# Performance work log

Measured on AMD Instinct MI355X. Metric: run time of the kernel, lower is better.

Reference implementation:

```python
import jax, jax.numpy as jnp
import numpy as np

B, N1, N2, C2, K = 8, 2048, 128, 256, 3
D_POS, H0, H1 = 32, 512, 1024


def setup_inputs() -> dict:
    key = jax.random.key(0)
    ks = jax.random.split(key, 14)
    return {
        "xyz1": jax.random.normal(ks[0], (B, N1, 3), jnp.float32),
        "xyz2": jax.random.normal(ks[1], (B, N2, 3), jnp.float32),
        "feat2": jax.random.normal(ks[2], (B, N2, C2), jnp.float32),
        "lrf2": jax.random.normal(ks[3], (B, N2, 3, 3), jnp.float32),
        "w_pos": jax.random.normal(ks[4], (D_POS, 4), jnp.float32) * 0.1,
        "pos_scale": jax.random.uniform(ks[5], (D_POS,), jnp.float32, 0.5, 1.5),
        "pos_bias": jax.random.normal(ks[6], (D_POS,), jnp.float32) * 0.1,
        "w0": jax.random.normal(ks[7], (H0, C2 + D_POS), jnp.float32) * 0.05,
        "s0": jax.random.uniform(ks[8], (H0,), jnp.float32, 0.5, 1.5),
        "b0": jax.random.normal(ks[9], (H0,), jnp.float32) * 0.1,
        "w1": jax.random.normal(ks[10], (H1, H0), jnp.float32) * 0.04,
        "s1": jax.random.uniform(ks[11], (H1,), jnp.float32, 0.5, 1.5),
        "b1": jax.random.normal(ks[12], (H1,), jnp.float32) * 0.1,
        "k": K,
    }


def reference(xyz1, xyz2, feat2, lrf2, w_pos, pos_scale, pos_bias,
              w0, s0, b0, w1, s1, b1, k):
    Bb = xyz1.shape[0]
    # --- get_dists: full pairwise sqrt-distance matrix (B, N1, N2) ---
    d2 = (jnp.sum(xyz1 * xyz1, -1)[:, :, None]
          + jnp.sum(xyz2 * xyz2, -1)[:, None, :]
          - 2.0 * jnp.einsum('bmc,bnc->bmn', xyz1, xyz2))
    dists = jnp.sqrt(jnp.where(d2 < 0, 1e-7, d2))
    # --- k-NN: smallest k in ascending order (== torch.sort then slice) ---
    _, inds = jax.lax.top_k(-dists, k)                    # (B, N1, k)
    bidx = jnp.arange(Bb)[:, None, None]
    feat_nb = feat2[bidx, inds]                           # (B, N1, k, C2)
    close = xyz2[bidx, inds]                              # (B, N1, k, 3)
    lrf_nb = lrf2[bidx, inds]                             # (B, N1, k, 3, 3)
    # --- geometric angle embedding ---
    rel = xyz1[:, :, None, :] - close                     # (B, N1, k, 3)
    rel_norm = jnp.linalg.norm(rel, axis=-1)              # (B, N1, k)
    unit = rel / jnp.maximum(rel_norm, 1e-12)[..., None]  # F.normalize eps
    angle = jnp.einsum('bnkij,bnkj->bnki', lrf_nb, unit)  # (B, N1, k, 3)
    rp = jnp.concatenate([rel_norm[..., None], angle], -1)  # (B, N1, k, 4)
    # --- posembed: 1x1 Conv2d (no bias) + folded BN + LeakyReLU(0.2) ---
    pos = jax.nn.leaky_relu(
        jnp.einsum('bnkc,oc->bnko', rp, w_pos) * pos_scale + pos_bias, 0.2)
    # --- backbone: two 1x1 convs with folded BN + ReLU ---
    x = jnp.concatenate([feat_nb, pos], -1)               # (B, N1, k, C2+32)
    h0 = jax.nn.relu(jnp.einsum('bnkc,oc->bnko', x, w0) * s0 + b0)
    h1 = jax.nn.relu(jnp.einsum('bnkc,oc->bnko', h0, w1) * s1 + b1)
    # --- sum over neighbors, return (B, C_out, N1) like torch ---
    return jnp.transpose(jnp.sum(h1, axis=2), (0, 2, 1))
```

## Files before the change

kernel.cpp:

```cpp
#include <hip/hip_runtime.h>


typedef unsigned short u16;
typedef __bf16 bf16x8 __attribute__((ext_vector_type(8)));
typedef float f32x4 __attribute__((ext_vector_type(4)));
typedef u16 u16x4 __attribute__((ext_vector_type(4)));
typedef u16 u16x8 __attribute__((ext_vector_type(8)));

#define BQ 8
#define N1Q 2048
#define N2Q 128
#define C2Q 256
#define DPOS 32
#define H0Q 512
#define H1Q 1024
#define NQ (BQ * N1Q)

#define WS_W0F 0u
#define WS_W0P 262144u
#define WS_W1 294912u
#define WS_F2B 1343488u
#define WS_F 1867776u
#define WS_H0 3964928u
#define WS_POS 54296576u
#define WS_IDX 57442304u

__device__ __forceinline__ u16 f2bf(float f) {
  unsigned int u = __builtin_bit_cast(unsigned int, f);
  return (u16)((u + 0x7FFFu + ((u >> 16) & 1u)) >> 16);
}

__device__ __forceinline__ void load16_lds(const void* g, void* l) {
  __builtin_amdgcn_global_load_lds(
      (const __attribute__((address_space(1))) unsigned int*)g,
      (__attribute__((address_space(3))) unsigned int*)l, 16, 0, 0);
}

__global__ void convert_inputs(const float* __restrict__ w0,
                               const float* __restrict__ w1,
                               const float* __restrict__ feat2,
                               u16* __restrict__ w0f, u16* __restrict__ w0p,
                               u16* __restrict__ w1b, u16* __restrict__ f2b) {
  int i = blockIdx.x * 256 + threadIdx.x;
  if (i < 131072) {
    int h = i >> 8, c = i & 255;
    w0f[i] = f2bf(w0[h * 288 + c]);
  } else if (i < 147456) {
    int j = i - 131072;
    int h = j >> 5, c = j & 31;
    w0p[j] = f2bf(w0[h * 288 + 256 + c]);
  } else if (i < 671744) {
    int j = i - 147456;
    w1b[j] = f2bf(w1[j]);
  } else {
    int j = i - 671744;
    f2b[j] = f2bf(feat2[j]);
  }
}

__global__ __launch_bounds__(256, 2) void fgemm(const u16* __restrict__ A,
                                                const u16* __restrict__ W,
                                                float* __restrict__ F) {
  __shared__ alignas(16) u16 As[128 * 32];
  __shared__ alignas(16) u16 Bs[128 * 32];
  const int m0 = (blockIdx.x >> 2) * 128, n0 = (blockIdx.x & 3) * 128;
  const int t = threadIdx.x;
  const int wv = t >> 6, lane = t & 63;
  const int wm = wv >> 1, wn = wv & 1;
  const int quad = lane >> 4, cc = lane & 15;
  const int srow = lane & 15, skc = quad * 8;
  f32x4 acc[4][4] = {};

  for (int k0 = 0; k0 < 256; k0 += 32) {
#pragma unroll
    for (int i = 0; i < 2; i++) {
      int g = i * 4 + wv;
      load16_lds(A + (size_t)(m0 + g * 16 + srow) * 256 + k0 + skc,
                 (char*)As + g * 1024 + (lane << 4));
      load16_lds(W + (size_t)(n0 + g * 16 + srow) * 256 + k0 + skc,
                 (char*)Bs + g * 1024 + (lane << 4));
    }
    __syncthreads();
    bf16x8 af[4], bf[4];
#pragma unroll
    for (int mt = 0; mt < 4; mt++)
      af[mt] = *(const bf16x8*)((const char*)As + (wm * 4 + mt) * 1024 + (lane << 4));
#pragma unroll
    for (int nt = 0; nt < 4; nt++)
      bf[nt] = *(const bf16x8*)((const char*)Bs + (wn * 4 + nt) * 1024 + (lane << 4));
#pragma unroll
    for (int mt = 0; mt < 4; mt++)
#pragma unroll
      for (int nt = 0; nt < 4; nt++)
        acc[mt][nt] = __builtin_amdgcn_mfma_f32_16x16x32_bf16(
            af[mt], bf[nt], acc[mt][nt], 0, 0, 0);
    __syncthreads();
  }

#pragma unroll
  for (int nt = 0; nt < 4; nt++) {
    int gn = n0 + wn * 64 + nt * 16 + cc;
#pragma unroll
    for (int mt = 0; mt < 4; mt++) {
      int gm = m0 + wm * 64 + mt * 16 + quad * 4;
#pragma unroll
      for (int r = 0; r < 4; r++)
        F[(size_t)(gm + r) * H0Q + gn] = acc[mt][nt][r];
    }
  }
}

__global__ __launch_bounds__(512, 2) void knn_pos(
    const float* __restrict__ xyz1, const float* __restrict__ xyz2,
    const float* __restrict__ lrf2, const float* __restrict__ w_pos,
    const float* __restrict__ pscale, const float* __restrict__ pbias,
    u16* __restrict__ posw, int* __restrict__ idxw) {
  __shared__ float xyz2s[N2Q * 3];
  __shared__ float n2s[N2Q];
  __shared__ float lrfs[N2Q * 9];
  __shared__ float wps[DPOS * 4];
  __shared__ float pss[DPOS];
  __shared__ float pbs[DPOS];
  __shared__ float candd[128 * 13];
  __shared__ int candi[128 * 13];
  __shared__ int idxb[384];

  const int t = threadIdx.x;
  const int qb = blockIdx.x * 128;
  const int b = qb >> 11;

  for (int i = t; i < N2Q * 3; i += 512) xyz2s[i] = xyz2[b * N2Q * 3 + i];
  for (int i = t; i < N2Q * 9; i += 512) lrfs[i] = lrf2[b * N2Q * 9 + i];
  if (t < DPOS * 4) wps[t] = w_pos[t];
  if (t < DPOS) { pss[t] = pscale[t]; pbs[t] = pbias[t]; }
  __syncthreads();
  if (t < N2Q) {
    float x = xyz2s[t * 3], y = xyz2s[t * 3 + 1], z = xyz2s[t * 3 + 2];
    n2s[t] = x * x + y * y + z * z;
  }
  __syncthreads();

  {
    const int ql = t >> 2, qt = t & 3;
    const int q = qb + ql;
    const float px = xyz1[q * 3], py = xyz1[q * 3 + 1], pz = xyz1[q * 3 + 2];
    const float pn = px * px + py * py + pz * pz;
    float d0 = 1e30f, d1 = 1e30f, d2v = 1e30f;
    int i0 = 0, i1 = 0, i2 = 0;
    const int ibeg = qt * 32;
    for (int i = ibeg; i < ibeg + 32; i++) {
      float dt = px * xyz2s[i * 3] + py * xyz2s[i * 3 + 1] + pz * xyz2s[i * 3 + 2];
      float d = pn + n2s[i] - 2.f * dt;
      if (d < d0) {
        d2v = d1; i2 = i1; d1 = d0; i1 = i0; d0 = d; i0 = i;
      } else if (d < d1) {
        d2v = d1; i2 = i1; d1 = d; i1 = i;
      } else if (d < d2v) {
        d2v = d; i2 = i;
      }
    }
    int base = ql * 13 + qt * 3;
    candd[base] = d0;      candi[base] = i0;
    candd[base + 1] = d1;  candi[base + 1] = i1;
    candd[base + 2] = d2v; candi[base + 2] = i2;
  }
  __syncthreads();

  if (t < 128) {
    float d0 = 1e30f, d1 = 1e30f, d2v = 1e30f;
    int i0 = 0, i1 = 0, i2 = 0;
    int base = t * 13;
#pragma unroll
    for (int c = 0; c < 12; c++) {
      float d = candd[base + c];
      int id = candi[base + c];
      if (d < d0) {
        d2v = d1; i2 = i1; d1 = d0; i1 = i0; d0 = d; i0 = id;
      } else if (d < d1) {
        d2v = d1; i2 = i1; d1 = d; i1 = id;
      } else if (d < d2v) {
        d2v = d; i2 = id;
      }
    }
    idxb[t] = i0;
    idxb[128 + t] = i1;
    idxb[256 + t] = i2;
  }
  __syncthreads();

  if (t < 384) {
    const int j = t >> 7, ql = t & 127;
    const int q = qb + ql;
    const float px = xyz1[q * 3], py = xyz1[q * 3 + 1], pz = xyz1[q * 3 + 2];
    const int id = idxb[j * 128 + ql];
    float rx = px - xyz2s[id * 3];
    float ry = py - xyz2s[id * 3 + 1];
    float rz = pz - xyz2s[id * 3 + 2];
    float rn = sqrtf(rx * rx + ry * ry + rz * rz);
    float inv = 1.f / fmaxf(rn, 1e-12f);
    float ux = rx * inv, uy = ry * inv, uz = rz * inv;
    const float* L = lrfs + id * 9;
    float a0 = L[0] * ux + L[1] * uy + L[2] * uz;
    float a1 = L[3] * ux + L[4] * uy + L[5] * uz;
    float a2 = L[6] * ux + L[7] * uy + L[8] * uz;
    const size_t row = (size_t)j * NQ + q;
    idxw[row] = id;
#pragma unroll
    for (int c = 0; c < 4; c++) {
      u16x8 chunk;
#pragma unroll
      for (int e = 0; e < 8; e++) {
        int o = c * 8 + e;
        float v = wps[o * 4] * rn + wps[o * 4 + 1] * a0 + wps[o * 4 + 2] * a1 +
                  wps[o * 4 + 3] * a2;
        v = v * pss[o] + pbs[o];
        v = (v >= 0.f) ? v : 0.2f * v;
        chunk[e] = f2bf(v);
      }
      *(u16x8*)(posw + row * 32 + c * 8) = chunk;
    }
  }
}

__global__ __launch_bounds__(256, 4) void h0_kernel(
    const u16* __restrict__ posw, const int* __restrict__ idxw,
    const u16* __restrict__ w0p, const float* __restrict__ F,
    const float* __restrict__ s0, const float* __restrict__ b0,
    u16* __restrict__ H0) {
  const int t = threadIdx.x;
  const int wv = t >> 6, lane = t & 63;
  const int quad = lane >> 4, cc = lane & 15;
  const int r0 = (blockIdx.x * 4 + wv) * 16;

  const int r = r0 + cc;
  const int q = r & (NQ - 1);
  const int bb = q >> 11;
  const int idv = idxw[r];
  const float* Fr = F + ((size_t)(bb * N2Q + idv)) * H0Q;
  u16* Hr = H0 + (size_t)r * H0Q;

  const bf16x8 afr = *(const bf16x8*)(posw + (size_t)r * 32 + quad * 8);
  const f32x4 zf = {};

#pragma unroll 4
  for (int nt = 0; nt < 32; nt++) {
    const bf16x8 bfr = *(const bf16x8*)(w0p + (nt * 16 + cc) * 32 + quad * 8);
    f32x4 acc = __builtin_amdgcn_mfma_f32_16x16x32_bf16(bfr, afr, zf, 0, 0, 0);
    const int hb = nt * 16 + quad * 4;
    const f32x4 sv = *(const f32x4*)(s0 + hb);
    const f32x4 bv = *(const f32x4*)(b0 + hb);
    const f32x4 fv = *(const f32x4*)(Fr + hb);
    u16x4 o4;
#pragma unroll
    for (int e = 0; e < 4; e++) {
      float h = (fv[e] + acc[e]) * sv[e] + bv[e];
      h = h > 0.f ? h : 0.f;
      o4[e] = f2bf(h);
    }
    *(u16x4*)(Hr + hb) = o4;
  }
}

__global__ __launch_bounds__(512, 2) void gemm2(const u16* __restrict__ A,
                                                const u16* __restrict__ W,
                                                const float* __restrict__ s,
                                                const float* __restrict__ bz,
                                                float* __restrict__ out) {
  __shared__ alignas(16) u16 As[3][128 * 64];
  __shared__ alignas(16) u16 Bs[3][256 * 64];
  const int id = blockIdx.x;
  const int xcd = id & 7, g = id >> 3;
  const int m0 = (xcd * 16 + (g >> 2)) * 128;
  const int n0 = (g & 3) * 256;
  const int t = threadIdx.x;
  const int wv = t >> 6, lane = t & 63;
  const int wm = wv >> 2, wn = wv & 3;
  const int quad = lane >> 4, cc = lane & 15;
  const int lr = lane & 15, lk = (lane >> 4) * 8;

  const size_t aOff = (size_t)(m0 + wv * 16 + lr) * 512 + lk;
  const size_t bOff = (size_t)(n0 + wv * 32 + lr) * 512 + lk;

  float sv[4], bv[4];
#pragma unroll
  for (int nt = 0; nt < 4; nt++) {
    int gn = n0 + wn * 64 + nt * 16 + cc;
    sv[nt] = s[gn];
    bv[nt] = bz[gn];
  }

  auto stage = [&](int kt, int bi) {
    const u16* Ap = A + (size_t)(kt >> 3) * ((size_t)NQ * H0Q) + ((kt & 7) << 6);
    const u16* Wp = W + ((kt & 7) << 6);
    char* ab = (char*)As[bi] + (lane << 4);
    char* bb = (char*)Bs[bi] + (lane << 4);
    load16_lds(Ap + aOff, ab + wv * 1024);
    load16_lds(Ap + aOff + 32, ab + (8 + wv) * 1024);
    load16_lds(Wp + bOff, bb + (wv * 2) * 1024);
    load16_lds(Wp + bOff + (size_t)16 * 512, bb + (wv * 2 + 1) * 1024);
    load16_lds(Wp + bOff + 32, bb + (16 + wv * 2) * 1024);
    load16_lds(Wp + bOff + (size_t)16 * 512 + 32, bb + (16 + wv * 2 + 1) * 1024);
  };

  f32x4 sum[4][4] = {};
  f32x4 acc[4][4] = {};

  auto tile = [&](int bi, int ktStage) {
    bf16x8 af[2][4], bf[2][4];
    const char* ab = (const char*)As[bi] + (lane << 4);
    const char* bb = (const char*)Bs[bi] + (lane << 4);
#pragma unroll
    for (int kk = 0; kk < 2; kk++)
#pragma unroll
      for (int mt = 0; mt < 4; mt++)
        af[kk][mt] = *(const bf16x8*)(ab + (kk * 8 + wm * 4 + mt) * 1024);
#pragma unroll
    for (int kk = 0; kk < 2; kk++)
#pragma unroll
      for (int nt = 0; nt < 4; nt++)
        bf[kk][nt] = *(const bf16x8*)(bb + (kk * 16 + wn * 4 + nt) * 1024);
    asm volatile("s_waitcnt lgkmcnt(0)" ::: "memory");
    __builtin_amdgcn_s_barrier();
    if (ktStage >= 0) stage(ktStage, bi);
    __builtin_amdgcn_s_setprio(1);
#pragma unroll
    for (int kk = 0; kk < 2; kk++)
#pragma unroll
      for (int mt = 0; mt < 4; mt++)
#pragma unroll
        for (int nt = 0; nt < 4; nt++)
          acc[mt][nt] = __builtin_amdgcn_mfma_f32_16x16x32_bf16(
              af[kk][mt], bf[kk][nt], acc[mt][nt], 0, 0, 0);
    __builtin_amdgcn_s_setprio(0);
  };

  auto fold = [&]() {
#pragma unroll
    for (int mt = 0; mt < 4; mt++)
#pragma unroll
      for (int nt = 0; nt < 4; nt++) {
#pragma unroll
        for (int r = 0; r < 4; r++) {
          float h = acc[mt][nt][r] * sv[nt] + bv[nt];
          sum[mt][nt][r] += (h > 0.f ? h : 0.f);
        }
        acc[mt][nt] = f32x4{};
      }
  };

  stage(0, 0);
  stage(1, 1);
  stage(2, 2);

#pragma unroll 3
  for (int kt = 0; kt < 21; kt++) {
    asm volatile("s_waitcnt vmcnt(12)" ::: "memory");
    __builtin_amdgcn_s_barrier();
    tile(kt % 3, kt + 3);
    if ((kt & 7) == 7) fold();
  }
  asm volatile("s_waitcnt vmcnt(12)" ::: "memory");
  __builtin_amdgcn_s_barrier();
  tile(0, -1);
  asm volatile("s_waitcnt vmcnt(6)" ::: "memory");
  __builtin_amdgcn_s_barrier();
  tile(1, -1);
  asm volatile("s_waitcnt vmcnt(0)" ::: "memory");
  __builtin_amdgcn_s_barrier();
  tile(2, -1);
  fold();

#pragma unroll
  for (int nt = 0; nt < 4; nt++) {
    int gn = n0 + wn * 64 + nt * 16 + cc;
#pragma unroll
    for (int mt = 0; mt < 4; mt++) {
      int gm = m0 + wm * 64 + mt * 16 + quad * 4;
#pragma unroll
      for (int r = 0; r < 4; r++) {
        int q = gm + r;
        out[((size_t)(q >> 11) * H1Q + gn) * N1Q + (q & 2047)] = sum[mt][nt][r];
      }
    }
  }
}

extern "C" void kernel_launch(void* const* d_in, const int* in_sizes, int n_in,
                              void* d_out, int out_size, void* d_ws,
                              size_t ws_size, hipStream_t stream) {
  const float* xyz1 = (const float*)d_in[0];
  const float* xyz2 = (const float*)d_in[1];
  const float* feat2 = (const float*)d_in[2];
  const float* lrf2 = (const float*)d_in[3];
  const float* w_pos = (const float*)d_in[4];
  const float* pscale = (const float*)d_in[5];
  const float* pbias = (const float*)d_in[6];
  const float* w0 = (const float*)d_in[7];
  const float* s0 = (const float*)d_in[8];
  const float* b0 = (const float*)d_in[9];
  const float* w1 = (const float*)d_in[10];
  const float* s1 = (const float*)d_in[11];
  const float* b1 = (const float*)d_in[12];
  float* out = (float*)d_out;

  char* ws = (char*)d_ws;
  u16* w0f = (u16*)(ws + WS_W0F);
  u16* w0p = (u16*)(ws + WS_W0P);
  u16* w1b = (u16*)(ws + WS_W1);
  u16* f2b = (u16*)(ws + WS_F2B);
  float* F = (float*)(ws + WS_F);
  u16* H0 = (u16*)(ws + WS_H0);
  u16* posw = (u16*)(ws + WS_POS);
  int* idxw = (int*)(ws + WS_IDX);

  convert_inputs<<<933888 / 256, 256, 0, stream>>>(w0, w1, feat2, w0f, w0p,
                                                   w1b, f2b);
  fgemm<<<32, 256, 0, stream>>>(f2b, w0f, F);
  knn_pos<<<128, 512, 0, stream>>>(xyz1, xyz2, lrf2, w_pos, pscale, pbias,
                                   posw, idxw);
  h0_kernel<<<768, 256, 0, stream>>>(posw, idxw, w0p, F, s0, b0, H0);
  gemm2<<<512, 512, 0, stream>>>(H0, w1b, s1, b1, out);
}
```

Before: 234.9 us.

## Stream gemm2 weights directly into registers and merge input conversion with kNN

In gemm2, the W1 operand is no longer staged through LDS. Each wave loads its B fragments straight from global memory into double-buffered registers, one k-step ahead, while the A operand keeps its triple-buffered LDS pipeline. This removes the B shared-memory buffers and their LDS reads, which should lower LDS pressure. The cost is duplicated global/L2 reads across waves and more vector registers. Separately, the weight and feature bf16 conversion is folded into the kNN/pos-embed kernel as extra blocks, removing one kernel launch.

```diff
diff --git a/kernel.cpp b/kernel.cpp
--- a/kernel.cpp
+++ b/kernel.cpp
@@ -36,85 +36,34 @@
       (__attribute__((address_space(3))) unsigned int*)l, 16, 0, 0);
 }
 
-__global__ void convert_inputs(const float* __restrict__ w0,
-                               const float* __restrict__ w1,
-                               const float* __restrict__ feat2,
-                               u16* __restrict__ w0f, u16* __restrict__ w0p,
-                               u16* __restrict__ w1b, u16* __restrict__ f2b) {
-  int i = blockIdx.x * 256 + threadIdx.x;
-  if (i < 131072) {
-    int h = i >> 8, c = i & 255;
-    w0f[i] = f2bf(w0[h * 288 + c]);
-  } else if (i < 147456) {
-    int j = i - 131072;
-    int h = j >> 5, c = j & 31;
-    w0p[j] = f2bf(w0[h * 288 + 256 + c]);
-  } else if (i < 671744) {
-    int j = i - 147456;
-    w1b[j] = f2bf(w1[j]);
-  } else {
-    int j = i - 671744;
-    f2b[j] = f2bf(feat2[j]);
-  }
-}
-
-__global__ __launch_bounds__(256, 2) void fgemm(const u16* __restrict__ A,
-                                                const u16* __restrict__ W,
-                                                float* __restrict__ F) {
-  __shared__ alignas(16) u16 As[128 * 32];
-  __shared__ alignas(16) u16 Bs[128 * 32];
-  const int m0 = (blockIdx.x >> 2) * 128, n0 = (blockIdx.x & 3) * 128;
-  const int t = threadIdx.x;
-  const int wv = t >> 6, lane = t & 63;
-  const int wm = wv >> 1, wn = wv & 1;
-  const int quad = lane >> 4, cc = lane & 15;
-  const int srow = lane & 15, skc = quad * 8;
-  f32x4 acc[4][4] = {};
-
-  for (int k0 = 0; k0 < 256; k0 += 32) {
-#pragma unroll
-    for (int i = 0; i < 2; i++) {
-      int g = i * 4 + wv;
-      load16_lds(A + (size_t)(m0 + g * 16 + srow) * 256 + k0 + skc,
-                 (char*)As + g * 1024 + (lane << 4));
-      load16_lds(W + (size_t)(n0 + g * 16 + srow) * 256 + k0 + skc,
-                 (char*)Bs + g * 1024 + (lane << 4));
-    }
-    __syncthreads();
-    bf16x8 af[4], bf[4];
-#pragma unroll
-    for (int mt = 0; mt < 4; mt++)
-      af[mt] = *(const bf16x8*)((const char*)As + (wm * 4 + mt) * 1024 + (lane << 4));
-#pragma unroll
-    for (int nt = 0; nt < 4; nt++)
-      bf[nt] = *(const bf16x8*)((const char*)Bs + (wn * 4 + nt) * 1024 + (lane << 4));
-#pragma unroll
-    for (int mt = 0; mt < 4; mt++)
-#pragma unroll
-      for (int nt = 0; nt < 4; nt++)
-        acc[mt][nt] = __builtin_amdgcn_mfma_f32_16x16x32_bf16(
-            af[mt], bf[nt], acc[mt][nt], 0, 0, 0);
-    __syncthreads();
-  }
-
-#pragma unroll
-  for (int nt = 0; nt < 4; nt++) {
-    int gn = n0 + wn * 64 + nt * 16 + cc;
-#pragma unroll
-    for (int mt = 0; mt < 4; mt++) {
-      int gm = m0 + wm * 64 + mt * 16 + quad * 4;
-#pragma unroll
-      for (int r = 0; r < 4; r++)
-        F[(size_t)(gm + r) * H0Q + gn] = acc[mt][nt][r];
-    }
-  }
-}
-
-__global__ __launch_bounds__(512, 2) void knn_pos(
+__global__ __launch_bounds__(512, 2) void prep(
     const float* __restrict__ xyz1, const float* __restrict__ xyz2,
     const float* __restrict__ lrf2, const float* __restrict__ w_pos,
     const float* __restrict__ pscale, const float* __restrict__ pbias,
-    u16* __restrict__ posw, int* __restrict__ idxw) {
+    const float* __restrict__ w0, const float* __restrict__ w1,
+    const float* __restrict__ feat2,
+    u16* __restrict__ posw, int* __restrict__ idxw,
+    u16* __restrict__ w0f, u16* __restrict__ w0p,
+    u16* __restrict__ w1b, u16* __restrict__ f2b) {
+  if (blockIdx.x >= 128) {
+    int i = (blockIdx.x - 128) * 512 + threadIdx.x;
+    if (i < 131072) {
+      int h = i >> 8, c = i & 255;
+      w0f[i] = f2bf(w0[h * 288 + c]);
+    } else if (i < 147456) {
+      int j = i - 131072;
+      int h = j >> 5, c = j & 31;
+      w0p[j] = f2bf(w0[h * 288 + 256 + c]);
+    } else if (i < 671744) {
+      int j = i - 147456;
+      w1b[j] = f2bf(w1[j]);
+    } else {
+      int j = i - 671744;
+      f2b[j] = f2bf(feat2[j]);
+    }
+    return;
+  }
+
   __shared__ float xyz2s[N2Q * 3];
   __shared__ float n2s[N2Q];
   __shared__ float lrfs[N2Q * 9];
@@ -222,6 +171,58 @@
   }
 }
 
+__global__ __launch_bounds__(256, 2) void fgemm(const u16* __restrict__ A,
+                                                const u16* __restrict__ W,
+                                                float* __restrict__ F) {
+  __shared__ alignas(16) u16 As[128 * 32];
+  __shared__ alignas(16) u16 Bs[128 * 32];
+  const int m0 = (blockIdx.x >> 2) * 128, n0 = (blockIdx.x & 3) * 128;
+  const int t = threadIdx.x;
+  const int wv = t >> 6, lane = t & 63;
+  const int wm = wv >> 1, wn = wv & 1;
+  const int quad = lane >> 4, cc = lane & 15;
+  const int srow = lane & 15, skc = quad * 8;
+  f32x4 acc[4][4] = {};
+
+  for (int k0 = 0; k0 < 256; k0 += 32) {
+#pragma unroll
+    for (int i = 0; i < 2; i++) {
+      int g = i * 4 + wv;
+      load16_lds(A + (size_t)(m0 + g * 16 + srow) * 256 + k0 + skc,
+                 (char*)As + g * 1024 + (lane << 4));
+      load16_lds(W + (size_t)(n0 + g * 16 + srow) * 256 + k0 + skc,
+                 (char*)Bs + g * 1024 + (lane << 4));
+    }
+    __syncthreads();
+    bf16x8 af[4], bf[4];
+#pragma unroll
+    for (int mt = 0; mt < 4; mt++)
+      af[mt] = *(const bf16x8*)((const char*)As + (wm * 4 + mt) * 1024 + (lane << 4));
+#pragma unroll
+    for (int nt = 0; nt < 4; nt++)
+      bf[nt] = *(const bf16x8*)((const char*)Bs + (wn * 4 + nt) * 1024 + (lane << 4));
+#pragma unroll
+    for (int mt = 0; mt < 4; mt++)
+#pragma unroll
+      for (int nt = 0; nt < 4; nt++)
+        acc[mt][nt] = __builtin_amdgcn_mfma_f32_16x16x32_bf16(
+            af[mt], bf[nt], acc[mt][nt], 0, 0, 0);
+    __syncthreads();
+  }
+
+#pragma unroll
+  for (int nt = 0; nt < 4; nt++) {
+    int gn = n0 + wn * 64 + nt * 16 + cc;
+#pragma unroll
+    for (int mt = 0; mt < 4; mt++) {
+      int gm = m0 + wm * 64 + mt * 16 + quad * 4;
+#pragma unroll
+      for (int r = 0; r < 4; r++)
+        F[(size_t)(gm + r) * H0Q + gn] = acc[mt][nt][r];
+    }
+  }
+}
+
 __global__ __launch_bounds__(256, 4) void h0_kernel(
     const u16* __restrict__ posw, const int* __restrict__ idxw,
     const u16* __restrict__ w0p, const float* __restrict__ F,
@@ -267,7 +268,6 @@
                                                 const float* __restrict__ bz,
                                                 float* __restrict__ out) {
   __shared__ alignas(16) u16 As[3][128 * 64];
-  __shared__ alignas(16) u16 Bs[3][256 * 64];
   const int id = blockIdx.x;
   const int xcd = id & 7, g = id >> 3;
   const int m0 = (xcd * 16 + (g >> 2)) * 128;
@@ -276,10 +276,13 @@
   const int wv = t >> 6, lane = t & 63;
   const int wm = wv >> 2, wn = wv & 3;
   const int quad = lane >> 4, cc = lane & 15;
-  const int lr = lane & 15, lk = (lane >> 4) * 8;
+  const int lr = lane & 15, lk = quad * 8;
 
   const size_t aOff = (size_t)(m0 + wv * 16 + lr) * 512 + lk;
-  const size_t bOff = (size_t)(n0 + wv * 32 + lr) * 512 + lk;
+  const u16* Wrow[4];
+#pragma unroll
+  for (int nt = 0; nt < 4; nt++)
+    Wrow[nt] = W + (size_t)(n0 + wn * 64 + nt * 16 + cc) * 512 + quad * 8;
 
   float sv[4], bv[4];
 #pragma unroll
@@ -288,51 +291,31 @@
     sv[nt] = s[gn];
     bv[nt] = bz[gn];
   }
-
-  auto stage = [&](int kt, int bi) {
+#pragma unroll
+  for (int nt = 0; nt < 4; nt++) {
+    float a = sv[nt], c = bv[nt];
+    asm volatile("" : "+v"(a), "+v"(c));
+    sv[nt] = a; bv[nt] = c;
+  }
+
+  auto stageA = [&](int kt) {
     const u16* Ap = A + (size_t)(kt >> 3) * ((size_t)NQ * H0Q) + ((kt & 7) << 6);
-    const u16* Wp = W + ((kt & 7) << 6);
-    char* ab = (char*)As[bi] + (lane << 4);
-    char* bb = (char*)Bs[bi] + (lane << 4);
+    char* ab = (char*)As[kt % 3] + (lane << 4);
     load16_lds(Ap + aOff, ab + wv * 1024);
     load16_lds(Ap + aOff + 32, ab + (8 + wv) * 1024);
-    load16_lds(Wp + bOff, bb + (wv * 2) * 1024);
-    load16_lds(Wp + bOff + (size_t)16 * 512, bb + (wv * 2 + 1) * 1024);
-    load16_lds(Wp + bOff + 32, bb + (16 + wv * 2) * 1024);
-    load16_lds(Wp + bOff + (size_t)16 * 512 + 32, bb + (16 + wv * 2 + 1) * 1024);
+  };
+
+  auto loadB = [&](int kt, bf16x8 bf[2][4]) {
+    const int k0 = (kt & 7) << 6;
+#pragma unroll
+    for (int kk = 0; kk < 2; kk++)
+#pragma unroll
+      for (int nt = 0; nt < 4; nt++)
+        bf[kk][nt] = *(const bf16x8*)(Wrow[nt] + k0 + kk * 32);
   };
 
   f32x4 sum[4][4] = {};
   f32x4 acc[4][4] = {};
-
-  auto tile = [&](int bi, int ktStage) {
-    bf16x8 af[2][4], bf[2][4];
-    const char* ab = (const char*)As[bi] + (lane << 4);
-    const char* bb = (const char*)Bs[bi] + (lane << 4);
-#pragma unroll
-    for (int kk = 0; kk < 2; kk++)
-#pragma unroll
-      for (int mt = 0; mt < 4; mt++)
-        af[kk][mt] = *(const bf16x8*)(ab + (kk * 8 + wm * 4 + mt) * 1024);
-#pragma unroll
-    for (int kk = 0; kk < 2; kk++)
-#pragma unroll
-      for (int nt = 0; nt < 4; nt++)
-        bf[kk][nt] = *(const bf16x8*)(bb + (kk * 16 + wn * 4 + nt) * 1024);
-    asm volatile("s_waitcnt lgkmcnt(0)" ::: "memory");
-    __builtin_amdgcn_s_barrier();
-    if (ktStage >= 0) stage(ktStage, bi);
-    __builtin_amdgcn_s_setprio(1);
-#pragma unroll
-    for (int kk = 0; kk < 2; kk++)
-#pragma unroll
-      for (int mt = 0; mt < 4; mt++)
-#pragma unroll
-        for (int nt = 0; nt < 4; nt++)
-          acc[mt][nt] = __builtin_amdgcn_mfma_f32_16x16x32_bf16(
-              af[kk][mt], bf[kk][nt], acc[mt][nt], 0, 0, 0);
-    __builtin_amdgcn_s_setprio(0);
-  };
 
   auto fold = [&]() {
 #pragma unroll
@@ -348,27 +331,43 @@
       }
   };
 
-  stage(0, 0);
-  stage(1, 1);
-  stage(2, 2);
-
-#pragma unroll 3
-  for (int kt = 0; kt < 21; kt++) {
+  bf16x8 bfA[2][4], bfB[2][4];
+  stageA(0);
+  stageA(1);
+  stageA(2);
+  loadB(0, bfA);
+
+  auto step = [&](int kt, bf16x8 bfCur[2][4], bf16x8 bfNxt[2][4]) {
     asm volatile("s_waitcnt vmcnt(12)" ::: "memory");
     __builtin_amdgcn_s_barrier();
-    tile(kt % 3, kt + 3);
+    bf16x8 af[2][4];
+    const char* ab = (const char*)As[kt % 3] + (lane << 4);
+#pragma unroll
+    for (int kk = 0; kk < 2; kk++)
+#pragma unroll
+      for (int mt = 0; mt < 4; mt++)
+        af[kk][mt] = *(const bf16x8*)(ab + (kk * 8 + wm * 4 + mt) * 1024);
+    asm volatile("s_waitcnt lgkmcnt(0)" ::: "memory");
+    __builtin_amdgcn_s_barrier();
+    if (kt + 3 < 24) stageA(kt + 3);
+    if (kt + 1 < 24) loadB(kt + 1, bfNxt);
+    __builtin_amdgcn_s_setprio(1);
+#pragma unroll
+    for (int kk = 0; kk < 2; kk++)
+#pragma unroll
+      for (int mt = 0; mt < 4; mt++)
+#pragma unroll
+        for (int nt = 0; nt < 4; nt++)
+          acc[mt][nt] = __builtin_amdgcn_mfma_f32_16x16x32_bf16(
+              af[kk][mt], bfCur[kk][nt], acc[mt][nt], 0, 0, 0);
+    __builtin_amdgcn_s_setprio(0);
     if ((kt & 7) == 7) fold();
-  }
-  asm volatile("s_waitcnt vmcnt(12)" ::: "memory");
-  __builtin_amdgcn_s_barrier();
-  tile(0, -1);
-  asm volatile("s_waitcnt vmcnt(6)" ::: "memory");
-  __builtin_amdgcn_s_barrier();
-  tile(1, -1);
-  asm volatile("s_waitcnt vmcnt(0)" ::: "memory");
-  __builtin_amdgcn_s_barrier();
-  tile(2, -1);
-  fold();
+  };
+
+  for (int kp = 0; kp < 12; kp++) {
+    step(2 * kp, bfA, bfB);
+    step(2 * kp + 1, bfB, bfA);
+  }
 
 #pragma unroll
   for (int nt = 0; nt < 4; nt++) {
@@ -413,11 +412,9 @@
   u16* posw = (u16*)(ws + WS_POS);
   int* idxw = (int*)(ws + WS_IDX);
 
-  convert_inputs<<<933888 / 256, 256, 0, stream>>>(w0, w1, feat2, w0f, w0p,
-                                                   w1b, f2b);
+  prep<<<1952, 512, 0, stream>>>(xyz1, xyz2, lrf2, w_pos, pscale, pbias, w0,
+                                 w1, feat2, posw, idxw, w0f, w0p, w1b, f2b);
   fgemm<<<32, 256, 0, stream>>>(f2b, w0f, F);
-  knn_pos<<<128, 512, 0, stream>>>(xyz1, xyz2, lrf2, w_pos, pscale, pbias,
-                                   posw, idxw);
   h0_kernel<<<768, 256, 0, stream>>>(posw, idxw, w0p, F, s0, b0, H0);
   gemm2<<<512, 512, 0, stream>>>(H0, w1b, s1, b1, out);
 }
```

Result: slower. 277.4 us (+18.1%).
